# Performance work log

Hardware: AMD Instinct MI355X
Metric: run time of the kernel (lower is better)

## Reference

```python
import jax, jax.numpy as jnp
import numpy as np

SEQ, BATCH, IN, HID, OUT = 4096, 64, 64, 256, 1


def setup_inputs() -> dict:
    key = jax.random.key(0)
    ks = jax.random.split(key, 7)
    s = 1.0 / np.sqrt(HID)  # torch GRU/Linear init scale
    return {
        "x": jax.random.normal(ks[0], (SEQ, BATCH, IN), dtype=jnp.float32),
        "w_ih": jax.random.uniform(ks[1], (3 * HID, IN), jnp.float32, -s, s),
        "w_hh": jax.random.uniform(ks[2], (3 * HID, HID), jnp.float32, -s, s),
        "b_ih": jax.random.uniform(ks[3], (3 * HID,), jnp.float32, -s, s),
        "b_hh": jax.random.uniform(ks[4], (3 * HID,), jnp.float32, -s, s),
        "fc_w": jax.random.uniform(ks[5], (OUT, HID), jnp.float32, -s, s),
        "fc_b": jax.random.uniform(ks[6], (OUT,), jnp.float32, -s, s),
    }


def _gru(x, w_ih, w_hh, b_ih, b_hh):
    # x: [S, B, I]. Precompute input-side gate projections in one big GEMM.
    xg = jnp.einsum("sbi,gi->sbg", x, w_ih) + b_ih  # [S, B, 3H]
    H = w_hh.shape[1]
    h0 = jnp.zeros((x.shape[1], H), x.dtype)

    def step(h, xt):
        hg = h @ w_hh.T + b_hh  # [B, 3H]
        xr, xz, xn = jnp.split(xt, 3, axis=-1)
        hr, hz, hn = jnp.split(hg, 3, axis=-1)
        r = jax.nn.sigmoid(xr + hr)
        z = jax.nn.sigmoid(xz + hz)
        n = jnp.tanh(xn + r * hn)  # torch GRU: r gates the hidden-side n term
        h_new = (1.0 - z) * n + z * h
        return h_new, h_new

    _, hs = jax.lax.scan(step, h0, xg)  # hs: [S, B, H]
    return hs


def reference(x, w_ih, w_hh, b_ih, b_hh, fc_w, fc_b):
    hs = _gru(x, w_ih, w_hh, b_ih, b_hh)  # [S, B, H]
    out = hs @ fc_w.T + fc_b  # [S, B, OUT]
    # original does .squeeze(0): no-op since S != 1
    return out
```

## Files before the change

### kernel.cpp

```cpp
#include <hip/hip_runtime.h>

#define SEQ  4096
#define NB   64
#define NI   64
#define NH   256

typedef short  bf16x8 __attribute__((ext_vector_type(8)));
typedef short  bf16x4 __attribute__((ext_vector_type(4)));
typedef short  bf16x2 __attribute__((ext_vector_type(2)));
typedef float  f32x4  __attribute__((ext_vector_type(4)));

__device__ __forceinline__ unsigned short f2bf(float f) {
    union { float f; unsigned u; } v; v.f = f;
    return (unsigned short)((v.u + 0x7fffu + ((v.u >> 16) & 1u)) >> 16);
}
__device__ __forceinline__ float bflo(int p) {
    union { int i; float f; } u; u.i = p << 16; return u.f;
}
__device__ __forceinline__ float bfhi(int p) {
    union { int i; float f; } u; u.i = p & 0xffff0000; return u.f;
}
__device__ __forceinline__ float fast_rcp(float x) { return __builtin_amdgcn_rcpf(x); }
__device__ __forceinline__ float sigm(float x) { return fast_rcp(1.f + __expf(-x)); }
__device__ __forceinline__ float tanh_(float x) {
    x = fminf(15.f, fmaxf(-15.f, x));
    float e = __expf(2.f * x);
    return (e - 1.f) * fast_rcp(e + 1.f);
}
__device__ __forceinline__ f32x4 mfma16(bf16x8 a, bf16x8 b, f32x4 c) {
    return __builtin_amdgcn_mfma_f32_16x16x32_bf16(a, b, c, 0, 0, 0);
}
__device__ __forceinline__ bf16x8 ldfrag(const float* p) {
    float4 a = *(const float4*)p;
    float4 b = *(const float4*)(p + 4);
    bf16x8 r;
    r[0] = (short)f2bf(a.x); r[1] = (short)f2bf(a.y);
    r[2] = (short)f2bf(a.z); r[3] = (short)f2bf(a.w);
    r[4] = (short)f2bf(b.x); r[5] = (short)f2bf(b.y);
    r[6] = (short)f2bf(b.z); r[7] = (short)f2bf(b.w);
    return r;
}

__global__ __launch_bounds__(512) void xg_pre(
        const float* __restrict__ x, const float* __restrict__ w_ih,
        const float* __restrict__ b_ih, short* __restrict__ xg,
        int t0, int ns)
{
    __shared__ short wihs[49152];
    __shared__ short axs[1024];

    const int tid = threadIdx.x, wv = tid >> 6, lane = tid & 63;
    const int nn = lane & 15, q = lane >> 4;

    float bb[6];
    #pragma unroll
    for (int i = 0; i < 6; ++i) {
        const int jb = wv + 8 * i;
        #pragma unroll
        for (int c = 0; c < 2; ++c) {
            bf16x8 f = ldfrag(w_ih + (jb * 16 + nn) * NI + c * 32 + q * 8);
            *(bf16x8*)(wihs + (jb * 2 + c) * 512 + lane * 8) = f;
        }
        bb[i] = b_ih[jb * 16 + nn];
    }
    __syncthreads();

    const int RT = ns * 4;
    for (int rt = blockIdx.x; rt < RT; rt += gridDim.x) {
        {
            const int f = 2 * tid, row = f >> 6, k = f & 63;
            float2 v = *(const float2*)(x + ((size_t)(t0 * 64) + rt * 16) * NI + f);
            bf16x2 s; s[0] = (short)f2bf(v.x); s[1] = (short)f2bf(v.y);
            *(bf16x2*)(axs + (k >> 5) * 512 + (((k >> 3) & 3) * 16 + row) * 8 + (k & 7)) = s;
        }
        __syncthreads();
        bf16x8 a0 = *(const bf16x8*)(axs + lane * 8);
        bf16x8 a1 = *(const bf16x8*)(axs + 512 + lane * 8);
        const int tl = rt >> 2, bc = rt & 3;
        #pragma unroll
        for (int i = 0; i < 6; ++i) {
            const int jb = wv + 8 * i;
            f32x4 acc = 0;
            acc = mfma16(a0, *(const bf16x8*)(wihs + (jb * 2 + 0) * 512 + lane * 8), acc);
            acc = mfma16(a1, *(const bf16x8*)(wihs + (jb * 2 + 1) * 512 + lane * 8), acc);
            bf16x4 v;
            #pragma unroll
            for (int m = 0; m < 4; ++m) v[m] = (short)f2bf(acc[m] + bb[i]);
            short* p = xg + ((((size_t)tl * 4 + bc) * 16 + (jb & 15)) * 64 + lane) * 12
                          + (jb >> 4) * 4;
            *(bf16x4*)p = v;
        }
        __syncthreads();
    }
}

__global__ __launch_bounds__(1024, 4) void gru_rec(
        const short* __restrict__ xg,
        const float* __restrict__ w_hh,
        const float* __restrict__ b_hh,
        const float* __restrict__ fc_w,
        const float* __restrict__ fc_b,
        float* __restrict__ out,
        float* __restrict__ hcar,
        int t0, int ns)
{
    __shared__ short wlds[65536];
    __shared__ short abuf[8192];
    __shared__ float fcred[512];
    __shared__ float oring[2048];

    const int tid = threadIdx.x, wv = tid >> 6, lane = tid & 63;
    const int nn = lane & 15, q = lane >> 4;
    const int bc = blockIdx.x, bbase = bc * 16;

    bf16x8 wr[8], wz[8];
    #pragma unroll
    for (int c = 0; c < 8; ++c)
        wr[c] = ldfrag(w_hh + (0 * NH + wv * 16 + nn) * NH + c * 32 + q * 8);
    #pragma unroll
    for (int c = 0; c < 8; ++c)
        wz[c] = ldfrag(w_hh + (1 * NH + wv * 16 + nn) * NH + c * 32 + q * 8);
    #pragma unroll
    for (int c = 0; c < 8; ++c) {
        bf16x8 f = ldfrag(w_hh + (2 * NH + wv * 16 + nn) * NH + c * 32 + q * 8);
        *(bf16x8*)(wlds + (wv * 8 + c) * 512 + lane * 8) = f;
    }
    const float bmr = b_hh[0 * NH + wv * 16 + nn];
    const float bmz = b_hh[1 * NH + wv * 16 + nn];
    const float bhn = b_hh[2 * NH + wv * 16 + nn];
    const float fcw = fc_w[wv * 16 + nn];
    const float fcb = fc_b[0];

    f32x4 hp = 0;
    if (t0 == 0) {
        ((int4*)abuf)[tid] = make_int4(0, 0, 0, 0);
    } else {
        #pragma unroll
        for (int m = 0; m < 4; ++m)
            hp[m] = hcar[(size_t)(bbase + q * 4 + m) * NH + wv * 16 + nn];
        const int f = tid * 4, b = f >> 8, k0 = f & 255;
        float4 v = *(const float4*)(hcar + (size_t)(bbase + b) * NH + k0);
        bf16x4 s; s[0] = (short)f2bf(v.x); s[1] = (short)f2bf(v.y);
        s[2] = (short)f2bf(v.z); s[3] = (short)f2bf(v.w);
        *(bf16x4*)(abuf + (k0 >> 5) * 512 + (((k0 >> 3) & 3) * 16 + b) * 8 + (k0 & 7)) = s;
    }

    const int j = wv * 16 + nn;
    const int koff = (j >> 5) * 512 + ((j >> 3) & 3) * 128 + (j & 7) + q * 32;
    const short* xgp = xg + ((size_t)(bc * 16 + wv) * 64 + lane) * 12;
    __syncthreads();

    for (int t = 0; t < ns; ++t) {
        const int cur = t & 1, nxt = cur ^ 1;

        int2 gx = *(const int2*)(xgp);
        int2 gz = *(const int2*)(xgp + 4);
        int2 gn = *(const int2*)(xgp + 8);
        xgp += 49152;

        if ((t & 63) == 1 && t >= 65) {
            const int s0 = t - 65, buf = (s0 >> 6) & 1;
            out[(size_t)(t0 + s0 + (tid >> 4)) * NB + bbase + (tid & 15)] =
                oring[buf * 1024 + (tid >> 4) * 16 + (tid & 15)];
        }

        f32x4 ar = 0, az = 0, an = 0;
        const short* ab = abuf + cur * 4096;
        #pragma unroll
        for (int c = 0; c < 8; ++c) {
            bf16x8 av = *(const bf16x8*)(ab + c * 512 + lane * 8);
            ar = mfma16(av, wr[c], ar);
            az = mfma16(av, wz[c], az);
            bf16x8 wn = *(const bf16x8*)(wlds + (wv * 8 + c) * 512 + lane * 8);
            an = mfma16(av, wn, an);
        }

        const float xr[4] = { bflo(gx.x), bfhi(gx.x), bflo(gx.y), bfhi(gx.y) };
        const float xz[4] = { bflo(gz.x), bfhi(gz.x), bflo(gz.y), bfhi(gz.y) };
        const float xn[4] = { bflo(gn.x), bfhi(gn.x), bflo(gn.y), bfhi(gn.y) };

        short* hw = abuf + nxt * 4096 + koff;
        f32x4 pf;
        #pragma unroll
        for (int m = 0; m < 4; ++m) {
            float r_ = sigm(ar[m] + bmr + xr[m]);
            float z_ = sigm(az[m] + bmz + xz[m]);
            float n_ = tanh_(fmaf(r_, an[m] + bhn, xn[m]));
            float h_ = n_ + z_ * (hp[m] - n_);
            hp[m] = h_;
            hw[m * 8] = (short)f2bf(h_);
            pf[m] = h_ * fcw;
        }
        #pragma unroll
        for (int d = 1; d < 16; d <<= 1) {
            pf[0] += __shfl_xor(pf[0], d);
            pf[1] += __shfl_xor(pf[1], d);
            pf[2] += __shfl_xor(pf[2], d);
            pf[3] += __shfl_xor(pf[3], d);
        }
        if (nn == 0)
            *(f32x4*)(fcred + cur * 256 + wv * 16 + q * 4) = pf;

        if (t > 0 && wv == (t & 15)) {
            const int s = t - 1, wg = lane >> 4, b = lane & 15;
            const float* fr = fcred + (s & 1) * 256 + b;
            float v = fr[wg * 16] + fr[(wg + 4) * 16] +
                      fr[(wg + 8) * 16] + fr[(wg + 12) * 16];
            v += __shfl_xor(v, 16);
            v += __shfl_xor(v, 32);
            if (lane < 16)
                oring[((s >> 6) & 1) * 1024 + (s & 63) * 16 + lane] = v + fcb;
        }
        __syncthreads();
    }

    if (wv == (ns & 15)) {
        const int s = ns - 1, wg = lane >> 4, b = lane & 15;
        const float* fr = fcred + (s & 1) * 256 + b;
        float v = fr[wg * 16] + fr[(wg + 4) * 16] +
                  fr[(wg + 8) * 16] + fr[(wg + 12) * 16];
        v += __shfl_xor(v, 16);
        v += __shfl_xor(v, 32);
        if (lane < 16)
            oring[((s >> 6) & 1) * 1024 + (s & 63) * 16 + lane] = v + fcb;
    }
    __syncthreads();
    {
        const int s0 = ns - 64, buf = (s0 >> 6) & 1;
        out[(size_t)(t0 + s0 + (tid >> 4)) * NB + bbase + (tid & 15)] =
            oring[buf * 1024 + (tid >> 4) * 16 + (tid & 15)];
    }
    #pragma unroll
    for (int m = 0; m < 4; ++m)
        hcar[(size_t)(bbase + q * 4 + m) * NH + wv * 16 + nn] = hp[m];
}

extern "C" void kernel_launch(void* const* d_in, const int* in_sizes, int n_in,
                              void* d_out, int out_size, void* d_ws, size_t ws_size,
                              hipStream_t stream) {
    (void)in_sizes; (void)n_in; (void)out_size;
    const float* x    = (const float*)d_in[0];
    const float* w_ih = (const float*)d_in[1];
    const float* w_hh = (const float*)d_in[2];
    const float* b_ih = (const float*)d_in[3];
    const float* b_hh = (const float*)d_in[4];
    const float* fc_w = (const float*)d_in[5];
    const float* fc_b = (const float*)d_in[6];
    float* out  = (float*)d_out;
    float* hcar = (float*)d_ws;
    short* xg   = (short*)((char*)d_ws + 65536);

    const size_t per_step = (size_t)NB * 3 * NH * 2;
    long avail = (long)ws_size - 65536;
    int spc = 64;
    if (avail >= (long)per_step * 64) {
        spc = (int)((avail / (long)per_step) / 64) * 64;
        if (spc > SEQ) spc = SEQ;
    }
    for (int t0 = 0; t0 < SEQ; t0 += spc) {
        int ns = (SEQ - t0 < spc) ? (SEQ - t0) : spc;
        xg_pre<<<dim3(512), dim3(512), 0, stream>>>(x, w_ih, b_ih, xg, t0, ns);
        gru_rec<<<dim3(4), dim3(1024), 0, stream>>>(xg, w_hh, b_hh, fc_w, fc_b,
                                                    out, hcar, t0, ns);
    }
}
```

Baseline: 7.966 ms.

## Fold r/z hidden biases into xg, compute FC via MFMA, split xg into gate planes

The input-projection kernel drops its LDS staging, holds the W_ih fragments in registers, loads x fragments straight from global memory, and writes each gate to its own plane. It also folds b_hh for the r and z gates into the precomputed bias. The recurrent kernel removes the per-step shuffle reduction for the final linear layer. Instead, one rotating wave runs extra MFMAs against a zero-padded fc_w tile in LDS, the output ring shrinks to 32-step chunks, and the r/z bias adds leave the critical path. In exchange, the FC now reads bf16 hidden state, and the chosen wave runs more MFMAs in the step that owns the FC.

```diff
diff --git a/kernel.cpp b/kernel.cpp
--- a/kernel.cpp
+++ b/kernel.cpp
@@ -7,7 +7,6 @@
 
 typedef short  bf16x8 __attribute__((ext_vector_type(8)));
 typedef short  bf16x4 __attribute__((ext_vector_type(4)));
-typedef short  bf16x2 __attribute__((ext_vector_type(2)));
 typedef float  f32x4  __attribute__((ext_vector_type(4)));
 
 __device__ __forceinline__ unsigned short f2bf(float f) {
@@ -41,61 +40,46 @@
     return r;
 }
 
-__global__ __launch_bounds__(512) void xg_pre(
+__global__ __launch_bounds__(1024) void xg_pre(
         const float* __restrict__ x, const float* __restrict__ w_ih,
-        const float* __restrict__ b_ih, short* __restrict__ xg,
-        int t0, int ns)
+        const float* __restrict__ b_ih, const float* __restrict__ b_hh,
+        short* __restrict__ xg, size_t plane, int t0, int ns)
 {
-    __shared__ short wihs[49152];
-    __shared__ short axs[1024];
-
     const int tid = threadIdx.x, wv = tid >> 6, lane = tid & 63;
     const int nn = lane & 15, q = lane >> 4;
-
-    float bb[6];
-    #pragma unroll
-    for (int i = 0; i < 6; ++i) {
-        const int jb = wv + 8 * i;
-        #pragma unroll
-        for (int c = 0; c < 2; ++c) {
-            bf16x8 f = ldfrag(w_ih + (jb * 16 + nn) * NI + c * 32 + q * 8);
-            *(bf16x8*)(wihs + (jb * 2 + c) * 512 + lane * 8) = f;
-        }
-        bb[i] = b_ih[jb * 16 + nn];
-    }
-    __syncthreads();
-
-    const int RT = ns * 4;
-    for (int rt = blockIdx.x; rt < RT; rt += gridDim.x) {
-        {
-            const int f = 2 * tid, row = f >> 6, k = f & 63;
-            float2 v = *(const float2*)(x + ((size_t)(t0 * 64) + rt * 16) * NI + f);
-            bf16x2 s; s[0] = (short)f2bf(v.x); s[1] = (short)f2bf(v.y);
-            *(bf16x2*)(axs + (k >> 5) * 512 + (((k >> 3) & 3) * 16 + row) * 8 + (k & 7)) = s;
-        }
-        __syncthreads();
-        bf16x8 a0 = *(const bf16x8*)(axs + lane * 8);
-        bf16x8 a1 = *(const bf16x8*)(axs + 512 + lane * 8);
-        const int tl = rt >> 2, bc = rt & 3;
-        #pragma unroll
-        for (int i = 0; i < 6; ++i) {
-            const int jb = wv + 8 * i;
-            f32x4 acc = 0;
-            acc = mfma16(a0, *(const bf16x8*)(wihs + (jb * 2 + 0) * 512 + lane * 8), acc);
-            acc = mfma16(a1, *(const bf16x8*)(wihs + (jb * 2 + 1) * 512 + lane * 8), acc);
+    const int jb = wv;
+
+    bf16x8 w[3][2];
+    float bias[3];
+    #pragma unroll
+    for (int g = 0; g < 3; ++g) {
+        const int row = g * NH + jb * 16 + nn;
+        w[g][0] = ldfrag(w_ih + row * NI + q * 8);
+        w[g][1] = ldfrag(w_ih + row * NI + 32 + q * 8);
+        bias[g] = b_ih[row] + (g < 2 ? b_hh[row] : 0.f);
+    }
+
+    const int NT = ns * 4;
+    for (int rt = blockIdx.x; rt < NT; rt += gridDim.x) {
+        const float* xr = x + ((size_t)t0 * NB + (size_t)rt * 16 + nn) * NI + q * 8;
+        bf16x8 a0 = ldfrag(xr);
+        bf16x8 a1 = ldfrag(xr + 32);
+        #pragma unroll
+        for (int g = 0; g < 3; ++g) {
+            f32x4 acc = {0.f, 0.f, 0.f, 0.f};
+            acc = mfma16(a0, w[g][0], acc);
+            acc = mfma16(a1, w[g][1], acc);
             bf16x4 v;
             #pragma unroll
-            for (int m = 0; m < 4; ++m) v[m] = (short)f2bf(acc[m] + bb[i]);
-            short* p = xg + ((((size_t)tl * 4 + bc) * 16 + (jb & 15)) * 64 + lane) * 12
-                          + (jb >> 4) * 4;
-            *(bf16x4*)p = v;
-        }
-        __syncthreads();
+            for (int m = 0; m < 4; ++m) v[m] = (short)f2bf(acc[m] + bias[g]);
+            *(bf16x4*)(xg + (size_t)g * plane +
+                       (((size_t)rt * 16 + jb) * 64 + lane) * 4) = v;
+        }
     }
 }
 
 __global__ __launch_bounds__(1024, 4) void gru_rec(
-        const short* __restrict__ xg,
+        const short* __restrict__ xg, size_t plane,
         const float* __restrict__ w_hh,
         const float* __restrict__ b_hh,
         const float* __restrict__ fc_w,
@@ -106,8 +90,8 @@
 {
     __shared__ short wlds[65536];
     __shared__ short abuf[8192];
-    __shared__ float fcred[512];
-    __shared__ float oring[2048];
+    __shared__ short fcwl[4096];
+    __shared__ float oring[1024];
 
     const int tid = threadIdx.x, wv = tid >> 6, lane = tid & 63;
     const int nn = lane & 15, q = lane >> 4;
@@ -125,13 +109,15 @@
         bf16x8 f = ldfrag(w_hh + (2 * NH + wv * 16 + nn) * NH + c * 32 + q * 8);
         *(bf16x8*)(wlds + (wv * 8 + c) * 512 + lane * 8) = f;
     }
-    const float bmr = b_hh[0 * NH + wv * 16 + nn];
-    const float bmz = b_hh[1 * NH + wv * 16 + nn];
+    if (wv < 8) {
+        bf16x8 f = 0;
+        if (nn == 0) f = ldfrag(fc_w + wv * 32 + q * 8);
+        *(bf16x8*)(fcwl + wv * 512 + lane * 8) = f;
+    }
     const float bhn = b_hh[2 * NH + wv * 16 + nn];
-    const float fcw = fc_w[wv * 16 + nn];
     const float fcb = fc_b[0];
 
-    f32x4 hp = 0;
+    f32x4 hp = {0.f, 0.f, 0.f, 0.f};
     if (t0 == 0) {
         ((int4*)abuf)[tid] = make_int4(0, 0, 0, 0);
     } else {
@@ -147,88 +133,84 @@
 
     const int j = wv * 16 + nn;
     const int koff = (j >> 5) * 512 + ((j >> 3) & 3) * 128 + (j & 7) + q * 32;
-    const short* xgp = xg + ((size_t)(bc * 16 + wv) * 64 + lane) * 12;
+    const short* xgp = xg + ((size_t)(bc * 16 + wv) * 64 + lane) * 4;
     __syncthreads();
 
     for (int t = 0; t < ns; ++t) {
         const int cur = t & 1, nxt = cur ^ 1;
 
         int2 gx = *(const int2*)(xgp);
-        int2 gz = *(const int2*)(xgp + 4);
-        int2 gn = *(const int2*)(xgp + 8);
-        xgp += 49152;
-
-        if ((t & 63) == 1 && t >= 65) {
-            const int s0 = t - 65, buf = (s0 >> 6) & 1;
-            out[(size_t)(t0 + s0 + (tid >> 4)) * NB + bbase + (tid & 15)] =
-                oring[buf * 1024 + (tid >> 4) * 16 + (tid & 15)];
-        }
-
-        f32x4 ar = 0, az = 0, an = 0;
+        int2 gz = *(const int2*)(xgp + plane);
+        int2 gn = *(const int2*)(xgp + 2 * plane);
+        xgp += 16384;
+
+        if ((t & 31) == 1 && t >= 33 && tid < 512) {
+            const int s0 = t - 33;
+            out[((size_t)(t0 + s0 + (tid >> 4))) * NB + bbase + (tid & 15)] =
+                oring[(((s0 >> 5) & 1) << 9) + (tid >> 4) * 16 + (tid & 15)];
+        }
+
+        const bool isfc = (t > 0) && (wv == (t & 15));
+        f32x4 ar = {0.f,0.f,0.f,0.f}, az = {0.f,0.f,0.f,0.f};
+        f32x4 an = {0.f,0.f,0.f,0.f}, afc = {0.f,0.f,0.f,0.f};
         const short* ab = abuf + cur * 4096;
         #pragma unroll
         for (int c = 0; c < 8; ++c) {
             bf16x8 av = *(const bf16x8*)(ab + c * 512 + lane * 8);
             ar = mfma16(av, wr[c], ar);
             az = mfma16(av, wz[c], az);
-            bf16x8 wn = *(const bf16x8*)(wlds + (wv * 8 + c) * 512 + lane * 8);
-            an = mfma16(av, wn, an);
-        }
-
-        const float xr[4] = { bflo(gx.x), bfhi(gx.x), bflo(gx.y), bfhi(gx.y) };
-        const float xz[4] = { bflo(gz.x), bfhi(gz.x), bflo(gz.y), bfhi(gz.y) };
-        const float xn[4] = { bflo(gn.x), bfhi(gn.x), bflo(gn.y), bfhi(gn.y) };
+            bf16x8 wnf = *(const bf16x8*)(wlds + (wv * 8 + c) * 512 + lane * 8);
+            an = mfma16(av, wnf, an);
+            if (isfc) {
+                bf16x8 ff = *(const bf16x8*)(fcwl + c * 512 + lane * 8);
+                afc = mfma16(av, ff, afc);
+            }
+        }
+        if (isfc && nn == 0) {
+            const int s = t - 1;
+            f32x4 v;
+            #pragma unroll
+            for (int m = 0; m < 4; ++m) v[m] = afc[m] + fcb;
+            *(f32x4*)(oring + (((s >> 5) & 1) << 9) + ((s & 31) << 4) + q * 4) = v;
+        }
+
+        const float xr4[4] = { bflo(gx.x), bfhi(gx.x), bflo(gx.y), bfhi(gx.y) };
+        const float xz4[4] = { bflo(gz.x), bfhi(gz.x), bflo(gz.y), bfhi(gz.y) };
+        const float xn4[4] = { bflo(gn.x), bfhi(gn.x), bflo(gn.y), bfhi(gn.y) };
 
         short* hw = abuf + nxt * 4096 + koff;
-        f32x4 pf;
         #pragma unroll
         for (int m = 0; m < 4; ++m) {
-            float r_ = sigm(ar[m] + bmr + xr[m]);
-            float z_ = sigm(az[m] + bmz + xz[m]);
-            float n_ = tanh_(fmaf(r_, an[m] + bhn, xn[m]));
+            float r_ = sigm(ar[m] + xr4[m]);
+            float z_ = sigm(az[m] + xz4[m]);
+            float n_ = tanh_(fmaf(r_, an[m] + bhn, xn4[m]));
             float h_ = n_ + z_ * (hp[m] - n_);
             hp[m] = h_;
             hw[m * 8] = (short)f2bf(h_);
-            pf[m] = h_ * fcw;
-        }
-        #pragma unroll
-        for (int d = 1; d < 16; d <<= 1) {
-            pf[0] += __shfl_xor(pf[0], d);
-            pf[1] += __shfl_xor(pf[1], d);
-            pf[2] += __shfl_xor(pf[2], d);
-            pf[3] += __shfl_xor(pf[3], d);
-        }
-        if (nn == 0)
-            *(f32x4*)(fcred + cur * 256 + wv * 16 + q * 4) = pf;
-
-        if (t > 0 && wv == (t & 15)) {
-            const int s = t - 1, wg = lane >> 4, b = lane & 15;
-            const float* fr = fcred + (s & 1) * 256 + b;
-            float v = fr[wg * 16] + fr[(wg + 4) * 16] +
-                      fr[(wg + 8) * 16] + fr[(wg + 12) * 16];
-            v += __shfl_xor(v, 16);
-            v += __shfl_xor(v, 32);
-            if (lane < 16)
-                oring[((s >> 6) & 1) * 1024 + (s & 63) * 16 + lane] = v + fcb;
         }
         __syncthreads();
     }
 
-    if (wv == (ns & 15)) {
-        const int s = ns - 1, wg = lane >> 4, b = lane & 15;
-        const float* fr = fcred + (s & 1) * 256 + b;
-        float v = fr[wg * 16] + fr[(wg + 4) * 16] +
-                  fr[(wg + 8) * 16] + fr[(wg + 12) * 16];
-        v += __shfl_xor(v, 16);
-        v += __shfl_xor(v, 32);
-        if (lane < 16)
-            oring[((s >> 6) & 1) * 1024 + (s & 63) * 16 + lane] = v + fcb;
+    if (wv == 0) {
+        const short* ab = abuf + (ns & 1) * 4096;
+        f32x4 afc = {0.f, 0.f, 0.f, 0.f};
+        #pragma unroll
+        for (int c = 0; c < 8; ++c)
+            afc = mfma16(*(const bf16x8*)(ab + c * 512 + lane * 8),
+                         *(const bf16x8*)(fcwl + c * 512 + lane * 8), afc);
+        if (nn == 0) {
+            const int s = ns - 1;
+            f32x4 v;
+            #pragma unroll
+            for (int m = 0; m < 4; ++m) v[m] = afc[m] + fcb;
+            *(f32x4*)(oring + (((s >> 5) & 1) << 9) + ((s & 31) << 4) + q * 4) = v;
+        }
     }
     __syncthreads();
-    {
-        const int s0 = ns - 64, buf = (s0 >> 6) & 1;
-        out[(size_t)(t0 + s0 + (tid >> 4)) * NB + bbase + (tid & 15)] =
-            oring[buf * 1024 + (tid >> 4) * 16 + (tid & 15)];
+    if (tid < 512) {
+        const int s0 = ns - 32;
+        out[((size_t)(t0 + s0 + (tid >> 4))) * NB + bbase + (tid & 15)] =
+            oring[(((s0 >> 5) & 1) << 9) + (tid >> 4) * 16 + (tid & 15)];
     }
     #pragma unroll
     for (int m = 0; m < 4; ++m)
@@ -259,8 +241,11 @@
     }
     for (int t0 = 0; t0 < SEQ; t0 += spc) {
         int ns = (SEQ - t0 < spc) ? (SEQ - t0) : spc;
-        xg_pre<<<dim3(512), dim3(512), 0, stream>>>(x, w_ih, b_ih, xg, t0, ns);
-        gru_rec<<<dim3(4), dim3(1024), 0, stream>>>(xg, w_hh, b_hh, fc_w, fc_b,
-                                                    out, hcar, t0, ns);
-    }
-}
+        size_t plane = (size_t)spc * 16384;
+        xg_pre<<<dim3(2048), dim3(1024), 0, stream>>>(x, w_ih, b_ih, b_hh,
+                                                      xg, plane, t0, ns);
+        gru_rec<<<dim3(4), dim3(1024), 0, stream>>>(xg, plane, w_hh, b_hh,
+                                                    fc_w, fc_b, out, hcar,
+                                                    t0, ns);
+    }
+}
```

Result: faster. 6.929 ms (-13.0%).
